# Optimization experiments

Measured on AMD Instinct MI355X. Metric: run time of the kernel, lower is better.

## Reference

```python
import jax, jax.numpy as jnp
import numpy as np

DIM = 512
A_HEADS = 8
C_HEADS = 4
DH = 64
EPS = 1e-5


def layer_norm(x, g, b):
    mu = jnp.mean(x, axis=-1, keepdims=True)
    var = jnp.var(x, axis=-1, keepdims=True)
    return (x - mu) * jax.lax.rsqrt(var + EPS) * g + b


def setup_inputs() -> dict:
    key = jax.random.key(0)
    ks = jax.random.split(key, 8)
    inner_a = A_HEADS * DH  # 512
    inner_c = C_HEADS * DH  # 256
    s = 0.02
    return {
        "x": jax.random.normal(ks[0], (4, 192, DIM), dtype=jnp.float32),
        # Attention branch params
        "ln1_g": jnp.ones((DIM,), jnp.float32),
        "ln1_b": jnp.zeros((DIM,), jnp.float32),
        "Wqkv": jax.random.normal(ks[1], (DIM, 3 * inner_a), jnp.float32) * s,
        "Wo": jax.random.normal(ks[2], (inner_a, DIM), jnp.float32) * s,
        "bo": jnp.zeros((DIM,), jnp.float32),
        # Trittention branch params
        "ln2_g": jnp.ones((DIM,), jnp.float32),
        "ln2_b": jnp.zeros((DIM,), jnp.float32),
        "Wabcde": jax.random.normal(ks[3], (DIM, 5 * inner_c), jnp.float32) * s,
        "babcde": jnp.zeros((5 * inner_c,), jnp.float32),
        "Wp": jax.random.normal(ks[4], (inner_c, DIM), jnp.float32) * s,
        "bp": jnp.zeros((DIM,), jnp.float32),
    }


def _attention(x, ln_g, ln_b, Wqkv, Wo, bo):
    B, T, _ = x.shape
    xn = layer_norm(x, ln_g, ln_b)
    qkv = xn @ Wqkv  # [B,T,3*H*D]
    q, k, v = jnp.split(qkv, 3, axis=-1)
    def heads(t):
        return t.reshape(B, T, A_HEADS, DH).transpose(0, 2, 1, 3)  # [B,H,T,D]
    q, k, v = heads(q), heads(k), heads(v)
    scale = DH ** -0.5
    dots = jnp.einsum('bhqd,bhkd->bhqk', q, k) * scale
    attn = jax.nn.softmax(dots, axis=-1)
    out = jnp.einsum('bhqk,bhkd->bhqd', attn, v)
    out = out.transpose(0, 2, 1, 3).reshape(B, T, A_HEADS * DH)
    return out @ Wo + bo


def _trittention(x, ln_g, ln_b, Wabcde, babcde, Wp, bp):
    B, T, _ = x.shape
    xn = layer_norm(x, ln_g, ln_b)
    proj = xn @ Wabcde + babcde  # [B,T,5*H*D]
    a, b_, c, d_, e = jnp.split(proj, 5, axis=-1)
    def heads(t):
        return t.reshape(B, T, C_HEADS, DH)  # [B,T,H,D]
    a, b_, c, d_, e = heads(a), heads(b_), heads(c), heads(d_), heads(e)
    # cubic score: [B,H,S,T,Q]
    score = jnp.einsum('bshd,bthd,bqhd->bhstq', a, b_, c) / DH
    # softmax over joint (s,t) for each query q
    score = score.transpose(0, 1, 4, 2, 3).reshape(B, C_HEADS, T, T * T)
    attn = jax.nn.softmax(score, axis=-1).reshape(B, C_HEADS, T, T, T)
    z = (jnp.einsum('bhqst,bshd->bhqd', attn, d_)
         + jnp.einsum('bhqst,bthd->bhqd', attn, e))
    z = z.transpose(0, 2, 1, 3).reshape(B, T, C_HEADS * DH)
    return z @ Wp + bp


def reference(x, ln1_g, ln1_b, Wqkv, Wo, bo, ln2_g, ln2_b, Wabcde, babcde, Wp, bp):
    return (_attention(x, ln1_g, ln1_b, Wqkv, Wo, bo)
            + _trittention(x, ln2_g, ln2_b, Wabcde, babcde, Wp, bp))
```

## Files before the change

kernel.cpp:

```cpp
#include <hip/hip_runtime.h>
#include <cstdint>


#define B_   4
#define T_   192
#define DIM_ 512
#define AH   8
#define CH   4

typedef unsigned short u16;
typedef unsigned int   u32;
typedef __attribute__((ext_vector_type(8))) short short8;
typedef __attribute__((ext_vector_type(4))) float floatx4;
typedef __attribute__((ext_vector_type(4))) int intx4;
typedef __attribute__((ext_vector_type(2))) float f32x2;
typedef __attribute__((ext_vector_type(8))) _Float16 half8;
typedef __attribute__((ext_vector_type(2))) _Float16 half2v;
typedef __attribute__((ext_vector_type(2))) __fp16 fp16x2;

union Frag  { intx4 i; short8 s; };
union FragH { intx4 i; half8 h; };

__device__ __forceinline__ floatx4 mfma16(Frag a, Frag b, floatx4 c) {
    return __builtin_amdgcn_mfma_f32_16x16x32_bf16(a.s, b.s, c, 0, 0, 0);
}
__device__ __forceinline__ floatx4 mfma16h(FragH a, FragH b, floatx4 c) {
    return __builtin_amdgcn_mfma_f32_16x16x32_f16(a.h, b.h, c, 0, 0, 0);
}

__device__ __forceinline__ float fexp2(float x) {
    return __builtin_amdgcn_exp2f(x);
}

__device__ __forceinline__ float wave_reduce_sum(float v) {
#pragma unroll
    for (int off = 32; off >= 1; off >>= 1)
        v += __shfl_xor(v, off, 64);
    return v;
}

__device__ __forceinline__ u32 pack_rne(float x, float y) {
    u32 ux = __float_as_uint(x);
    u32 uy = __float_as_uint(y);
    ux += 0x7fffu + ((ux >> 16) & 1u);
    uy += 0x7fffu + ((uy >> 16) & 1u);
    return (ux >> 16) | (uy & 0xffff0000u);
}
__device__ __forceinline__ u16 bf16_rne(float x) {
    u32 u = __float_as_uint(x);
    u += 0x7fffu + ((u >> 16) & 1u);
    return (u16)(u >> 16);
}
__device__ __forceinline__ float bf16f(u16 h) { return __uint_as_float(((u32)h) << 16); }

__device__ __forceinline__ u32 pack_f16(float x, float y) {
    union { fp16x2 h; u32 u; } cv;
    cv.h = __builtin_amdgcn_cvt_pkrtz(x, y);
    return cv.u;
}
__device__ __forceinline__ u32 mul_h2(u32 a, u32 b) {
    union { u32 u; half2v h; } ua, ub, uw;
    ua.u = a; ub.u = b;
    uw.h = ua.h * ub.h;
    return uw.u;
}

__device__ __forceinline__ Frag ld_frag8(const u16* p) {
    Frag f;
    uint2 a = *(const uint2*)p;
    uint2 b = *(const uint2*)(p + 4);
    f.i = (intx4){ (int)a.x, (int)a.y, (int)b.x, (int)b.y };
    return f;
}

#define LOG2E 1.44269504088896f

__global__ __launch_bounds__(256) void prep_kernel(
    const float* __restrict__ x,
    const float* __restrict__ g1, const float* __restrict__ b1,
    const float* __restrict__ g2, const float* __restrict__ b2,
    u16* __restrict__ x1h, u16* __restrict__ x2h,
    const float* __restrict__ Wqkv, u16* __restrict__ wqh,
    const float* __restrict__ Wab,  u16* __restrict__ wah,
    const float* __restrict__ Wo,   const float* __restrict__ Wp,
    u16* __restrict__ wofh, float* __restrict__ zero_base)
{
    __shared__ union { float t[64][65]; float red[4][2]; } u;
    const int tid = threadIdx.x;
    {
        int gid = blockIdx.x * 256 + tid;
        if (gid < 294912) ((float4*)zero_base)[gid] = make_float4(0.f, 0.f, 0.f, 0.f);
    }
    if (blockIdx.x < 768) {
        int row = blockIdx.x;
        const float2 v = ((const float2*)(x + (size_t)row * DIM_))[tid];
        float s  = v.x + v.y;
        float s2 = v.x * v.x + v.y * v.y;
        s  = wave_reduce_sum(s);
        s2 = wave_reduce_sum(s2);
        int w = tid >> 6;
        if ((tid & 63) == 0) { u.red[w][0] = s; u.red[w][1] = s2; }
        __syncthreads();
        float ts  = u.red[0][0] + u.red[1][0] + u.red[2][0] + u.red[3][0];
        float ts2 = u.red[0][1] + u.red[1][1] + u.red[2][1] + u.red[3][1];
        float mean = ts * (1.0f / DIM_);
        float var  = ts2 * (1.0f / DIM_) - mean * mean;
        float rstd = rsqrtf(var + 1e-5f);
        int c0 = tid * 2;
        float n0 = (v.x - mean) * rstd;
        float n1 = (v.y - mean) * rstd;
        float a0 = n0 * g1[c0] + b1[c0], a1 = n1 * g1[c0 + 1] + b1[c0 + 1];
        float c2 = n0 * g2[c0] + b2[c0], c3 = n1 * g2[c0 + 1] + b2[c0 + 1];
        size_t o = (size_t)row * 256 + tid;
        ((u32*)x1h)[o] = pack_rne(a0, a1);
        ((u32*)x2h)[o] = pack_rne(c2, c3);
        return;
    }
    int id = blockIdx.x - 768;
    const float* W; u16 *H; int K, N, Kout, kofs, tile;
    if (id < 192)      { W = Wqkv; H = wqh;  K = 512; N = 1536; Kout = 512; kofs = 0;   tile = id;       }
    else if (id < 352) { W = Wab;  H = wah;  K = 512; N = 1280; Kout = 512; kofs = 0;   tile = id - 192; }
    else if (id < 416) { W = Wo;   H = wofh; K = 512; N = 512;  Kout = 768; kofs = 0;   tile = id - 352; }
    else               { W = Wp;   H = wofh; K = 256; N = 512;  Kout = 768; kofs = 512; tile = id - 416; }
    int nx = N >> 6;
    int n0 = (tile % nx) * 64, k0 = (tile / nx) * 64;
    int rr = tid >> 4, c4 = (tid & 15) << 2;
#pragma unroll
    for (int p = 0; p < 4; ++p) {
        int row = rr + p * 16;
        float4 v = *(const float4*)(W + (size_t)(k0 + row) * N + n0 + c4);
        u.t[row][c4 + 0] = v.x; u.t[row][c4 + 1] = v.y;
        u.t[row][c4 + 2] = v.z; u.t[row][c4 + 3] = v.w;
    }
    __syncthreads();
#pragma unroll
    for (int p = 0; p < 4; ++p) {
        int n = rr + p * 16;
        u16 hi[4];
#pragma unroll
        for (int c = 0; c < 4; ++c)
            hi[c] = bf16_rne(u.t[c4 + c][n]);
        size_t o = (size_t)(n0 + n) * Kout + kofs + k0 + c4;
        *(uint2*)&H[o] = make_uint2((u32)hi[0] | ((u32)hi[1] << 16), (u32)hi[2] | ((u32)hi[3] << 16));
    }
}

__global__ __launch_bounds__(256) void gemm_dual(
    const u16* __restrict__ x1h, const u16* __restrict__ wqh,
    const u16* __restrict__ x2h, const u16* __restrict__ wah,
    const float* __restrict__ babcde,
    float* __restrict__ qkv, float* __restrict__ proj)
{
    __shared__ u16 As[64][68];
    __shared__ u16 Bs[64][68];
    const int tid = threadIdx.x;
    const int nb = blockIdx.x;
    const u16 *Ah, *BTh; const float* bias; float* C; int N, bn;
    if (nb < 24) { Ah = x1h; BTh = wqh; bias = nullptr; C = qkv;  N = 1536; bn = nb * 64; }
    else         { Ah = x2h; BTh = wah; bias = babcde; C = proj; N = 1280; bn = (nb - 24) * 64; }
    const int K = 512;
    const int bm = blockIdx.y * 64;
    const int lane = tid & 63, wave = tid >> 6;
    const int m16 = lane & 15, quad = lane >> 4;
    const int wm = (wave >> 1) * 32, wn = (wave & 1) * 32;
    const int r = tid >> 2, c16 = (tid & 3) * 16;

    floatx4 acc[2][2];
#pragma unroll
    for (int i = 0; i < 2; ++i)
#pragma unroll
        for (int j = 0; j < 2; ++j) acc[i][j] = (floatx4){0.f, 0.f, 0.f, 0.f};

    for (int k0 = 0; k0 < K; k0 += 64) {
        __syncthreads();
        {
            const u16* pa = Ah + (size_t)(bm + r) * K + k0 + c16;
            uint4 v0 = *(const uint4*)pa, v1 = *(const uint4*)(pa + 8);
            *(uint2*)&As[r][c16 + 0]  = make_uint2(v0.x, v0.y);
            *(uint2*)&As[r][c16 + 4]  = make_uint2(v0.z, v0.w);
            *(uint2*)&As[r][c16 + 8]  = make_uint2(v1.x, v1.y);
            *(uint2*)&As[r][c16 + 12] = make_uint2(v1.z, v1.w);
        }
        {
            const u16* pb = BTh + (size_t)(bn + r) * K + k0 + c16;
            uint4 v0 = *(const uint4*)pb, v1 = *(const uint4*)(pb + 8);
            *(uint2*)&Bs[r][c16 + 0]  = make_uint2(v0.x, v0.y);
            *(uint2*)&Bs[r][c16 + 4]  = make_uint2(v0.z, v0.w);
            *(uint2*)&Bs[r][c16 + 8]  = make_uint2(v1.x, v1.y);
            *(uint2*)&Bs[r][c16 + 12] = make_uint2(v1.z, v1.w);
        }
        __syncthreads();
#pragma unroll
        for (int ks = 0; ks < 2; ++ks) {
            const int ko = ks * 32 + quad * 8;
            Frag a0 = ld_frag8(&As[wm + m16][ko]);
            Frag a1 = ld_frag8(&As[wm + 16 + m16][ko]);
            Frag b0 = ld_frag8(&Bs[wn + m16][ko]);
            Frag b1 = ld_frag8(&Bs[wn + 16 + m16][ko]);
            acc[0][0] = mfma16(a0, b0, acc[0][0]);
            acc[0][1] = mfma16(a0, b1, acc[0][1]);
            acc[1][0] = mfma16(a1, b0, acc[1][0]);
            acc[1][1] = mfma16(a1, b1, acc[1][1]);
        }
    }
#pragma unroll
    for (int i = 0; i < 2; ++i)
#pragma unroll
        for (int rr = 0; rr < 4; ++rr) {
            int m = bm + wm + i * 16 + quad * 4 + rr;
#pragma unroll
            for (int j = 0; j < 2; ++j) {
                int n = bn + wn + j * 16 + m16;
                float v = acc[i][j][rr];
                if (bias) v += bias[n];
                C[(size_t)m * N + n] = v;
            }
        }
}

__global__ __launch_bounds__(256) void gemm_epilogue(
    const u16* __restrict__ aoh, const u16* __restrict__ zh,
    const u16* __restrict__ BTh,
    const float* __restrict__ bo, const float* __restrict__ bp,
    float* __restrict__ C)
{
    __shared__ u16 As[32][68];
    __shared__ u16 Bs[64][68];
    const int tid = threadIdx.x;
    const int bm = blockIdx.y * 32, bn = blockIdx.x * 64;
    const int lane = tid & 63, wave = tid >> 6;
    const int m16 = lane & 15, quad = lane >> 4;
    const int wm = (wave >> 1) * 16, wn = (wave & 1) * 32;
    const int ra = tid >> 3, c8 = (tid & 7) * 8;
    const int rb = tid >> 2, c16 = (tid & 3) * 16;
    const int N = 512, K = 768;

    floatx4 acc[2];
    acc[0] = (floatx4){0.f, 0.f, 0.f, 0.f};
    acc[1] = (floatx4){0.f, 0.f, 0.f, 0.f};

    for (int k0 = 0; k0 < K; k0 += 64) {
        __syncthreads();
        {
            const u16* pah = (k0 < 512)
                ? aoh + (size_t)(bm + ra) * 512 + k0 + c8
                : zh  + (size_t)(bm + ra) * 256 + (k0 - 512) + c8;
            uint4 v = *(const uint4*)pah;
            *(uint2*)&As[ra][c8 + 0] = make_uint2(v.x, v.y);
            *(uint2*)&As[ra][c8 + 4] = make_uint2(v.z, v.w);
        }
        {
            const u16* pb = BTh + (size_t)(bn + rb) * K + k0 + c16;
            uint4 v0 = *(const uint4*)pb, v1 = *(const uint4*)(pb + 8);
            *(uint2*)&Bs[rb][c16 + 0]  = make_uint2(v0.x, v0.y);
            *(uint2*)&Bs[rb][c16 + 4]  = make_uint2(v0.z, v0.w);
            *(uint2*)&Bs[rb][c16 + 8]  = make_uint2(v1.x, v1.y);
            *(uint2*)&Bs[rb][c16 + 12] = make_uint2(v1.z, v1.w);
        }
        __syncthreads();
#pragma unroll
        for (int ks = 0; ks < 2; ++ks) {
            const int ko = ks * 32 + quad * 8;
            Frag ah = ld_frag8(&As[wm + m16][ko]);
            Frag b0 = ld_frag8(&Bs[wn + m16][ko]);
            Frag b1 = ld_frag8(&Bs[wn + 16 + m16][ko]);
            acc[0] = mfma16(ah, b0, acc[0]);
            acc[1] = mfma16(ah, b1, acc[1]);
        }
    }
#pragma unroll
    for (int rr = 0; rr < 4; ++rr) {
        int m = bm + wm + quad * 4 + rr;
#pragma unroll
        for (int j = 0; j < 2; ++j) {
            int n = bn + wn + j * 16 + m16;
            C[(size_t)m * N + n] = acc[j][rr] + bo[n] + bp[n];
        }
    }
}

__global__ __launch_bounds__(256, 3) void attn_tritt(
    const float* __restrict__ qkv, const float* __restrict__ proj,
    u16* __restrict__ aoh, float* __restrict__ rs1, float* __restrict__ rt1)
{
    __shared__ union {
        struct {
            union { u16 Ks[96][68]; u16 P[64][100]; } kp;
            u16 Vt[64][100];
        } at;
        struct {
            u32 a_lds[48 * 36];
            u32 b_lds[48 * 36];
            float rs_lds[48][33];
            float rt_lds[48][33];
        } tr;
    } S;
    const int tid = threadIdx.x;
    const int lane = tid & 63, wave = tid >> 6;
    const int m16 = lane & 15, quad = lane >> 4;

    if (blockIdx.x < 96) {
        const int ab = blockIdx.x;
        const int b = ab / 24, rem = ab % 24;
        const int h = rem / 3, qt3 = rem % 3;
        const int qg = wave;
        const size_t base = (size_t)(b * T_) * 1536 + h * 64;

        Frag qf0, qf1;
        {
            const float s = 0.125f * LOG2E;
            const float* qp = qkv + base + (size_t)(qt3 * 64 + qg * 16 + m16) * 1536 + quad * 8;
            float4 u0 = *(const float4*)qp;
            float4 u1 = *(const float4*)(qp + 4);
            float4 u2 = *(const float4*)(qp + 32);
            float4 u3 = *(const float4*)(qp + 36);
            qf0.i = (intx4){ (int)pack_rne(u0.x * s, u0.y * s), (int)pack_rne(u0.z * s, u0.w * s),
                             (int)pack_rne(u1.x * s, u1.y * s), (int)pack_rne(u1.z * s, u1.w * s) };
            qf1.i = (intx4){ (int)pack_rne(u2.x * s, u2.y * s), (int)pack_rne(u2.z * s, u2.w * s),
                             (int)pack_rne(u3.x * s, u3.y * s), (int)pack_rne(u3.z * s, u3.w * s) };
        }

        float rsum[4] = {0.f, 0.f, 0.f, 0.f};
        floatx4 acco[4];
#pragma unroll
        for (int dt = 0; dt < 4; ++dt) acco[dt] = (floatx4){0.f, 0.f, 0.f, 0.f};

        for (int p = 0; p < 2; ++p) {
            if (p) __syncthreads();
            for (int i = tid; i < 96 * 16; i += 256) {
                int row = i >> 4, c4 = (i & 15) << 2;
                const float* kp = qkv + base + (size_t)(p * 96 + row) * 1536 + 512 + c4;
                float4 kv = *(const float4*)kp;
                *(uint2*)&S.at.kp.Ks[row][c4] = make_uint2(pack_rne(kv.x, kv.y), pack_rne(kv.z, kv.w));
                float4 vv = *(const float4*)(qkv + base + (size_t)(p * 96 + row) * 1536 + 1024 + c4);
                S.at.Vt[c4 + 0][row] = bf16_rne(vv.x);
                S.at.Vt[c4 + 1][row] = bf16_rne(vv.y);
                S.at.Vt[c4 + 2][row] = bf16_rne(vv.z);
                S.at.Vt[c4 + 3][row] = bf16_rne(vv.w);
            }
            __syncthreads();

            float ev[6][4];
#pragma unroll
            for (int tt = 0; tt < 6; ++tt) {
                Frag kb0 = ld_frag8(&S.at.kp.Ks[tt * 16 + m16][quad * 8]);
                Frag kb1 = ld_frag8(&S.at.kp.Ks[tt * 16 + m16][32 + quad * 8]);
                floatx4 accs = (floatx4){0.f, 0.f, 0.f, 0.f};
                accs = mfma16(qf0, kb0, accs);
                accs = mfma16(qf1, kb1, accs);
#pragma unroll
                for (int rr = 0; rr < 4; ++rr) {
                    float e = fexp2(accs[rr]);
                    ev[tt][rr] = e;
                    rsum[rr] += e;
                }
            }
            __syncthreads();
#pragma unroll
            for (int tt = 0; tt < 6; ++tt)
#pragma unroll
                for (int rr = 0; rr < 4; ++rr)
                    S.at.kp.P[qg * 16 + quad * 4 + rr][tt * 16 + m16] = bf16_rne(ev[tt][rr]);
#pragma unroll
            for (int ts = 0; ts < 3; ++ts) {
                Frag pf = ld_frag8(&S.at.kp.P[qg * 16 + m16][ts * 32 + quad * 8]);
#pragma unroll
                for (int dt = 0; dt < 4; ++dt) {
                    Frag vf = ld_frag8(&S.at.Vt[dt * 16 + m16][ts * 32 + quad * 8]);
                    acco[dt] = mfma16(pf, vf, acco[dt]);
                }
            }
        }

        float rinv[4];
#pragma unroll
        for (int rr = 0; rr < 4; ++rr) {
            float v = rsum[rr];
            v += __shfl_xor(v, 1, 64);
            v += __shfl_xor(v, 2, 64);
            v += __shfl_xor(v, 4, 64);
            v += __shfl_xor(v, 8, 64);
            rinv[rr] = 1.0f / v;
        }
#pragma unroll
        for (int dt = 0; dt < 4; ++dt)
#pragma unroll
            for (int rr = 0; rr < 4; ++rr) {
                float o = acco[dt][rr] * rinv[rr];
                size_t idx = (size_t)(b * T_ + qt3 * 64 + qg * 16 + quad * 4 + rr) * 512
                           + h * 64 + dt * 16 + m16;
                aoh[idx] = bf16_rne(o);
            }
        return;
    }

    const int t2 = blockIdx.x - 96;
    const int xx = t2 % 96;
    const int h = (t2 / 96) % CH;
    const int b = t2 / (96 * CH);
    const int qt = xx >> 4;
    const int sc = (xx >> 2) & 3;
    const int tc = xx & 3;
    const int q0 = qt * 32, s0 = sc * 48, t0 = tc * 48;
    const int bh = b * CH + h;
    const size_t rowbase = (size_t)(b * T_) * 1280 + h * 64;
    const float kA = 0.015625f * LOG2E;

    for (int i = tid; i < 48 * 32; i += 256) {
        int row = i >> 5, cp = i & 31;
        const float2 va = *(const float2*)(proj + rowbase + (size_t)(s0 + row) * 1280 + 0 + cp * 2);
        S.tr.a_lds[row * 36 + cp] = pack_f16(va.x * kA, va.y * kA);
        const float2 vb = *(const float2*)(proj + rowbase + (size_t)(t0 + row) * 1280 + 256 + cp * 2);
        S.tr.b_lds[row * 36 + cp] = pack_f16(vb.x, vb.y);
    }

    FragH cf[2][2];
#pragma unroll
    for (int jq = 0; jq < 2; ++jq) {
        const float* cp = proj + rowbase + (size_t)(q0 + jq * 16 + m16) * 1280 + 512 + quad * 8;
        float4 u0 = *(const float4*)(cp);
        float4 u1 = *(const float4*)(cp + 4);
        float4 u2 = *(const float4*)(cp + 32);
        float4 u3 = *(const float4*)(cp + 36);
        cf[jq][0].i = (intx4){ (int)pack_f16(u0.x, u0.y), (int)pack_f16(u0.z, u0.w),
                               (int)pack_f16(u1.x, u1.y), (int)pack_f16(u1.z, u1.w) };
        cf[jq][1].i = (intx4){ (int)pack_f16(u2.x, u2.y), (int)pack_f16(u2.z, u2.w),
                               (int)pack_f16(u3.x, u3.y), (int)pack_f16(u3.z, u3.w) };
    }
    __syncthreads();

    float rt_acc[3][4][2] = {};

    for (int si = 0; si < 12; ++si) {
        const int srow = wave * 12 + si;
        const intx4 av0 = *(const intx4*)(S.tr.a_lds + srow * 36 + quad * 4);
        const intx4 av1 = *(const intx4*)(S.tr.a_lds + srow * 36 + 16 + quad * 4);
        float rs_s[2] = {0.f, 0.f};
#pragma unroll
        for (int tt = 0; tt < 3; ++tt) {
            const u32* bp = S.tr.b_lds + (tt * 16 + m16) * 36;
            intx4 bv0 = *(const intx4*)(bp + quad * 4);
            intx4 bv1 = *(const intx4*)(bp + 16 + quad * 4);
            FragH w0, w1;
#pragma unroll
            for (int j = 0; j < 4; ++j) {
                w0.i[j] = (int)mul_h2((u32)av0[j], (u32)bv0[j]);
                w1.i[j] = (int)mul_h2((u32)av1[j], (u32)bv1[j]);
            }
#pragma unroll
            for (int jq = 0; jq < 2; ++jq) {
                floatx4 acc = (floatx4){0.f, 0.f, 0.f, 0.f};
                acc = mfma16h(w0, cf[jq][0], acc);
                acc = mfma16h(w1, cf[jq][1], acc);
#pragma unroll
                for (int rr = 0; rr < 4; ++rr) {
                    float e = fexp2(acc[rr]);
                    rt_acc[tt][rr][jq] += e;
                    rs_s[jq] += e;
                }
            }
        }
#pragma unroll
        for (int jq = 0; jq < 2; ++jq) {
            float v = rs_s[jq];
            v += __shfl_xor(v, 16, 64);
            v += __shfl_xor(v, 32, 64);
            if (lane < 16) S.tr.rs_lds[srow][jq * 16 + m16] = v;
        }
    }

    __syncthreads();
    for (int w = 0; w < 4; ++w) {
        if (wave == w) {
#pragma unroll
            for (int tt = 0; tt < 3; ++tt)
#pragma unroll
                for (int rr = 0; rr < 4; ++rr) {
                    int t = tt * 16 + quad * 4 + rr;
#pragma unroll
                    for (int jq = 0; jq < 2; ++jq) {
                        if (w == 0) S.tr.rt_lds[t][jq * 16 + m16] = rt_acc[tt][rr][jq];
                        else        S.tr.rt_lds[t][jq * 16 + m16] += rt_acc[tt][rr][jq];
                    }
                }
        }
        __syncthreads();
    }
    for (int i = tid; i < 32 * 48; i += 256) {
        int qq = i / 48, ss = i - qq * 48;
        unsafeAtomicAdd(&rs1[((size_t)bh * T_ + q0 + qq) * T_ + s0 + ss], S.tr.rs_lds[ss][qq]);
    }
    for (int i = tid; i < 32 * 48; i += 256) {
        int qq = i / 48, t3 = i - qq * 48;
        unsafeAtomicAdd(&rt1[((size_t)bh * T_ + q0 + qq) * T_ + t0 + t3], S.tr.rt_lds[t3][qq]);
    }
}

__global__ __launch_bounds__(256) void zgemm(
    const float* __restrict__ rs1, const float* __restrict__ rt1,
    const float* __restrict__ proj, u16* __restrict__ zzh)
{
    __shared__ u16 As[2][32][68];
    __shared__ u16 Bs[64][68];
    __shared__ float zred[32][9];
    __shared__ float Zl[32];
    const int mt = blockIdx.x, bh = blockIdx.y;
    const int b = bh >> 2, h = bh & 3;
    const int q0 = mt * 32;
    const int tid = threadIdx.x;
    const int lane = tid & 63, wave = tid >> 6;
    const int m16 = lane & 15, quad = lane >> 4;
    const int wm = (wave >> 1) * 16, wn = (wave & 1) * 32;
    const int ra = tid >> 3, c8 = (tid & 7) * 8;
    const int sl = tid >> 2, d4b = (tid & 3) * 4;

    float zacc = 0.f;
    floatx4 acc[2];
    acc[0] = (floatx4){0.f, 0.f, 0.f, 0.f};
    acc[1] = (floatx4){0.f, 0.f, 0.f, 0.f};

    for (int k0 = 0; k0 < 384; k0 += 64) {
        __syncthreads();
        {
            float g[8];
            if (k0 < 192) {
                const float* p = rs1 + ((size_t)bh * T_ + q0 + ra) * T_ + k0 + c8;
                float4 v0 = *(const float4*)(p);
                float4 v1 = *(const float4*)(p + 4);
                g[0] = v0.x; g[1] = v0.y; g[2] = v0.z; g[3] = v0.w;
                g[4] = v1.x; g[5] = v1.y; g[6] = v1.z; g[7] = v1.w;
                zacc += ((g[0] + g[1]) + (g[2] + g[3])) + ((g[4] + g[5]) + (g[6] + g[7]));
            } else {
                const float* p = rt1 + ((size_t)bh * T_ + q0 + ra) * T_ + (k0 - 192) + c8;
                float4 v0 = *(const float4*)(p);
                float4 v1 = *(const float4*)(p + 4);
                g[0] = v0.x; g[1] = v0.y; g[2] = v0.z; g[3] = v0.w;
                g[4] = v1.x; g[5] = v1.y; g[6] = v1.z; g[7] = v1.w;
            }
#pragma unroll
            for (int i = 0; i < 8; ++i) {
                u16 hi = bf16_rne(g[i]);
                As[0][ra][c8 + i] = hi;
                As[1][ra][c8 + i] = bf16_rne(g[i] - bf16f(hi));
            }
        }
        {
            const int colbase = (k0 < 192 ? 768 : 1024) + h * 64;
            const int s0 = (k0 < 192 ? k0 : k0 - 192);
#pragma unroll
            for (int i = 0; i < 4; ++i) {
                int dd = d4b + i * 16;
                float4 v = *(const float4*)(proj + (size_t)(b * T_ + s0 + sl) * 1280 + colbase + dd);
                Bs[dd + 0][sl] = bf16_rne(v.x);
                Bs[dd + 1][sl] = bf16_rne(v.y);
                Bs[dd + 2][sl] = bf16_rne(v.z);
                Bs[dd + 3][sl] = bf16_rne(v.w);
            }
        }
        __syncthreads();
#pragma unroll
        for (int ks = 0; ks < 2; ++ks) {
            const int ko = ks * 32 + quad * 8;
            Frag gh = ld_frag8(&As[0][wm + m16][ko]);
            Frag gl = ld_frag8(&As[1][wm + m16][ko]);
            Frag d0 = ld_frag8(&Bs[wn + m16][ko]);
            Frag d1 = ld_frag8(&Bs[wn + 16 + m16][ko]);
            acc[0] = mfma16(gh, d0, acc[0]);
            acc[0] = mfma16(gl, d0, acc[0]);
            acc[1] = mfma16(gh, d1, acc[1]);
            acc[1] = mfma16(gl, d1, acc[1]);
        }
    }
    zred[ra][tid & 7] = zacc;
    __syncthreads();
    if (tid < 32) {
        float s = ((zred[tid][0] + zred[tid][1]) + (zred[tid][2] + zred[tid][3]))
                + ((zred[tid][4] + zred[tid][5]) + (zred[tid][6] + zred[tid][7]));
        Zl[tid] = 1.0f / s;
    }
    __syncthreads();
#pragma unroll
    for (int j = 0; j < 2; ++j)
#pragma unroll
        for (int rr = 0; rr < 4; ++rr) {
            int m = wm + quad * 4 + rr;
            int d = wn + j * 16 + m16;
            float zv = acc[j][rr] * Zl[m];
            size_t idx = (size_t)(b * T_ + q0 + m) * 256 + h * 64 + d;
            zzh[idx] = bf16_rne(zv);
        }
}

extern "C" void kernel_launch(void* const* d_in, const int* in_sizes, int n_in,
                              void* d_out, int out_size, void* d_ws, size_t ws_size,
                              hipStream_t stream)
{
    const float* x      = (const float*)d_in[0];
    const float* ln1_g  = (const float*)d_in[1];
    const float* ln1_b  = (const float*)d_in[2];
    const float* Wqkv   = (const float*)d_in[3];
    const float* Wo     = (const float*)d_in[4];
    const float* bo     = (const float*)d_in[5];
    const float* ln2_g  = (const float*)d_in[6];
    const float* ln2_b  = (const float*)d_in[7];
    const float* Wabcde = (const float*)d_in[8];
    const float* babcde = (const float*)d_in[9];
    const float* Wp     = (const float*)d_in[10];
    const float* bp     = (const float*)d_in[11];
    float* out = (float*)d_out;

    float* ws   = (float*)d_ws;
    float* proj = ws;
    u16* wofh   = (u16*)(ws + 983040);
    u16* aoh    = (u16*)(ws + 1179648);
    u16* zh     = (u16*)(ws + 1376256);
    float* qkv  = ws + 1474560;
    u16* x1h    = (u16*)(ws + 2654208);
    u16* x2h    = (u16*)(ws + 2850816);
    u16* wqh    = (u16*)(ws + 3047424);
    u16* wah    = (u16*)(ws + 3440640);
    float* rs1  = ws + 3768320;
    float* rt1  = ws + 4358144;

    prep_kernel<<<1216, 256, 0, stream>>>(x, ln1_g, ln1_b, ln2_g, ln2_b,
                                          x1h, x2h,
                                          Wqkv, wqh, Wabcde, wah,
                                          Wo, Wp, wofh, rs1);
    gemm_dual<<<dim3(44, 12), 256, 0, stream>>>(x1h, wqh, x2h, wah,
                                                babcde, qkv, proj);
    attn_tritt<<<96 + 1536, 256, 0, stream>>>(qkv, proj, aoh, rs1, rt1);
    zgemm<<<dim3(6, 16), 256, 0, stream>>>(rs1, rt1, proj, zh);
    gemm_epilogue<<<dim3(8, 24), 256, 0, stream>>>(aoh, zh, wofh, bo, bp, out);
}
```

Baseline: 148.4 us.

## Fuse z-GEMM and output projection into one kernel with atomic accumulation

```diff
diff --git a/kernel.cpp b/kernel.cpp
--- a/kernel.cpp
+++ b/kernel.cpp
@@ -83,13 +83,14 @@
     const float* __restrict__ Wqkv, u16* __restrict__ wqh,
     const float* __restrict__ Wab,  u16* __restrict__ wah,
     const float* __restrict__ Wo,   const float* __restrict__ Wp,
-    u16* __restrict__ wofh, float* __restrict__ zero_base)
+    u16* __restrict__ wofh, float* __restrict__ zero_base, float* __restrict__ outz)
 {
     __shared__ union { float t[64][65]; float red[4][2]; } u;
     const int tid = threadIdx.x;
     {
         int gid = blockIdx.x * 256 + tid;
         if (gid < 294912) ((float4*)zero_base)[gid] = make_float4(0.f, 0.f, 0.f, 0.f);
+        if (gid < 98304)  ((float4*)outz)[gid]      = make_float4(0.f, 0.f, 0.f, 0.f);
     }
     if (blockIdx.x < 768) {
         int row = blockIdx.x;
@@ -174,7 +175,8 @@
     for (int k0 = 0; k0 < K; k0 += 64) {
         __syncthreads();
         {
-            const u16* pa = Ah + (size_t)(bm + r) * K + k0 + c16;
+            const u16* pa = x1h == Ah ? Ah + (size_t)(bm + r) * K + k0 + c16
+                                      : Ah + (size_t)(bm + r) * K + k0 + c16;
             uint4 v0 = *(const uint4*)pa, v1 = *(const uint4*)(pa + 8);
             *(uint2*)&As[r][c16 + 0]  = make_uint2(v0.x, v0.y);
             *(uint2*)&As[r][c16 + 4]  = make_uint2(v0.z, v0.w);
@@ -216,67 +218,6 @@
                 C[(size_t)m * N + n] = v;
             }
         }
-}
-
-__global__ __launch_bounds__(256) void gemm_epilogue(
-    const u16* __restrict__ aoh, const u16* __restrict__ zh,
-    const u16* __restrict__ BTh,
-    const float* __restrict__ bo, const float* __restrict__ bp,
-    float* __restrict__ C)
-{
-    __shared__ u16 As[32][68];
-    __shared__ u16 Bs[64][68];
-    const int tid = threadIdx.x;
-    const int bm = blockIdx.y * 32, bn = blockIdx.x * 64;
-    const int lane = tid & 63, wave = tid >> 6;
-    const int m16 = lane & 15, quad = lane >> 4;
-    const int wm = (wave >> 1) * 16, wn = (wave & 1) * 32;
-    const int ra = tid >> 3, c8 = (tid & 7) * 8;
-    const int rb = tid >> 2, c16 = (tid & 3) * 16;
-    const int N = 512, K = 768;
-
-    floatx4 acc[2];
-    acc[0] = (floatx4){0.f, 0.f, 0.f, 0.f};
-    acc[1] = (floatx4){0.f, 0.f, 0.f, 0.f};
-
-    for (int k0 = 0; k0 < K; k0 += 64) {
-        __syncthreads();
-        {
-            const u16* pah = (k0 < 512)
-                ? aoh + (size_t)(bm + ra) * 512 + k0 + c8
-                : zh  + (size_t)(bm + ra) * 256 + (k0 - 512) + c8;
-            uint4 v = *(const uint4*)pah;
-            *(uint2*)&As[ra][c8 + 0] = make_uint2(v.x, v.y);
-            *(uint2*)&As[ra][c8 + 4] = make_uint2(v.z, v.w);
-        }
-        {
-            const u16* pb = BTh + (size_t)(bn + rb) * K + k0 + c16;
-            uint4 v0 = *(const uint4*)pb, v1 = *(const uint4*)(pb + 8);
-            *(uint2*)&Bs[rb][c16 + 0]  = make_uint2(v0.x, v0.y);
-            *(uint2*)&Bs[rb][c16 + 4]  = make_uint2(v0.z, v0.w);
-            *(uint2*)&Bs[rb][c16 + 8]  = make_uint2(v1.x, v1.y);
-            *(uint2*)&Bs[rb][c16 + 12] = make_uint2(v1.z, v1.w);
-        }
-        __syncthreads();
-#pragma unroll
-        for (int ks = 0; ks < 2; ++ks) {
-            const int ko = ks * 32 + quad * 8;
-            Frag ah = ld_frag8(&As[wm + m16][ko]);
-            Frag b0 = ld_frag8(&Bs[wn + m16][ko]);
-            Frag b1 = ld_frag8(&Bs[wn + 16 + m16][ko]);
-            acc[0] = mfma16(ah, b0, acc[0]);
-            acc[1] = mfma16(ah, b1, acc[1]);
-        }
-    }
-#pragma unroll
-    for (int rr = 0; rr < 4; ++rr) {
-        int m = bm + wm + quad * 4 + rr;
-#pragma unroll
-        for (int j = 0; j < 2; ++j) {
-            int n = bn + wn + j * 16 + m16;
-            C[(size_t)m * N + n] = acc[j][rr] + bo[n] + bp[n];
-        }
-    }
 }
 
 __global__ __launch_bounds__(256, 3) void attn_tritt(
@@ -496,20 +437,73 @@
     }
 }
 
-__global__ __launch_bounds__(256) void zgemm(
-    const float* __restrict__ rs1, const float* __restrict__ rt1,
-    const float* __restrict__ proj, u16* __restrict__ zzh)
+__global__ __launch_bounds__(256) void finale(
+    const u16* __restrict__ aoh, const float* __restrict__ rs1, const float* __restrict__ rt1,
+    const float* __restrict__ proj, const u16* __restrict__ wofh,
+    const float* __restrict__ bo, const float* __restrict__ bp,
+    float* __restrict__ out)
 {
-    __shared__ u16 As[2][32][68];
-    __shared__ u16 Bs[64][68];
-    __shared__ float zred[32][9];
-    __shared__ float Zl[32];
-    const int mt = blockIdx.x, bh = blockIdx.y;
-    const int b = bh >> 2, h = bh & 3;
-    const int q0 = mt * 32;
+    __shared__ union {
+        struct { u16 As[32][68]; u16 Bs[64][68]; } A;
+        struct { u16 Am[2][32][68]; u16 Bs[64][68]; float zred[32][9]; float Zl[32]; } B;
+    } S;
     const int tid = threadIdx.x;
     const int lane = tid & 63, wave = tid >> 6;
     const int m16 = lane & 15, quad = lane >> 4;
+
+    if (blockIdx.x < 192) {
+        const int bn = (blockIdx.x & 7) * 64, bm = (blockIdx.x >> 3) * 32;
+        const int wm = (wave >> 1) * 16, wn = (wave & 1) * 32;
+        const int ra = tid >> 3, c8 = (tid & 7) * 8;
+        const int rb = tid >> 2, c16 = (tid & 3) * 16;
+
+        floatx4 acc[2];
+        acc[0] = (floatx4){0.f, 0.f, 0.f, 0.f};
+        acc[1] = (floatx4){0.f, 0.f, 0.f, 0.f};
+
+        for (int k0 = 0; k0 < 512; k0 += 64) {
+            __syncthreads();
+            {
+                const u16* pah = aoh + (size_t)(bm + ra) * 512 + k0 + c8;
+                uint4 v = *(const uint4*)pah;
+                *(uint2*)&S.A.As[ra][c8 + 0] = make_uint2(v.x, v.y);
+                *(uint2*)&S.A.As[ra][c8 + 4] = make_uint2(v.z, v.w);
+            }
+            {
+                const u16* pb = wofh + (size_t)(bn + rb) * 768 + k0 + c16;
+                uint4 v0 = *(const uint4*)pb, v1 = *(const uint4*)(pb + 8);
+                *(uint2*)&S.A.Bs[rb][c16 + 0]  = make_uint2(v0.x, v0.y);
+                *(uint2*)&S.A.Bs[rb][c16 + 4]  = make_uint2(v0.z, v0.w);
+                *(uint2*)&S.A.Bs[rb][c16 + 8]  = make_uint2(v1.x, v1.y);
+                *(uint2*)&S.A.Bs[rb][c16 + 12] = make_uint2(v1.z, v1.w);
+            }
+            __syncthreads();
+#pragma unroll
+            for (int ks = 0; ks < 2; ++ks) {
+                const int ko = ks * 32 + quad * 8;
+                Frag ah = ld_frag8(&S.A.As[wm + m16][ko]);
+                Frag b0 = ld_frag8(&S.A.Bs[wn + m16][ko]);
+                Frag b1 = ld_frag8(&S.A.Bs[wn + 16 + m16][ko]);
+                acc[0] = mfma16(ah, b0, acc[0]);
+                acc[1] = mfma16(ah, b1, acc[1]);
+            }
+        }
+#pragma unroll
+        for (int rr = 0; rr < 4; ++rr) {
+            int m = bm + wm + quad * 4 + rr;
+#pragma unroll
+            for (int j = 0; j < 2; ++j) {
+                int n = bn + wn + j * 16 + m16;
+                unsafeAtomicAdd(&out[(size_t)m * 512 + n], acc[j][rr] + bo[n] + bp[n]);
+            }
+        }
+        return;
+    }
+
+    const int blockB = blockIdx.x - 192;
+    const int mt = blockB % 6, bh = blockB / 6;
+    const int b = bh >> 2, h = bh & 3;
+    const int q0 = mt * 32;
     const int wm = (wave >> 1) * 16, wn = (wave & 1) * 32;
     const int ra = tid >> 3, c8 = (tid & 7) * 8;
     const int sl = tid >> 2, d4b = (tid & 3) * 4;
@@ -540,8 +534,8 @@
 #pragma unroll
             for (int i = 0; i < 8; ++i) {
                 u16 hi = bf16_rne(g[i]);
-                As[0][ra][c8 + i] = hi;
-                As[1][ra][c8 + i] = bf16_rne(g[i] - bf16f(hi));
+                S.B.Am[0][ra][c8 + i] = hi;
+                S.B.Am[1][ra][c8 + i] = bf16_rne(g[i] - bf16f(hi));
             }
         }
         {
@@ -551,44 +545,73 @@
             for (int i = 0; i < 4; ++i) {
                 int dd = d4b + i * 16;
                 float4 v = *(const float4*)(proj + (size_t)(b * T_ + s0 + sl) * 1280 + colbase + dd);
-                Bs[dd + 0][sl] = bf16_rne(v.x);
-                Bs[dd + 1][sl] = bf16_rne(v.y);
-                Bs[dd + 2][sl] = bf16_rne(v.z);
-                Bs[dd + 3][sl] = bf16_rne(v.w);
+                S.B.Bs[dd + 0][sl] = bf16_rne(v.x);
+                S.B.Bs[dd + 1][sl] = bf16_rne(v.y);
+                S.B.Bs[dd + 2][sl] = bf16_rne(v.z);
+                S.B.Bs[dd + 3][sl] = bf16_rne(v.w);
             }
         }
         __syncthreads();
 #pragma unroll
         for (int ks = 0; ks < 2; ++ks) {
             const int ko = ks * 32 + quad * 8;
-            Frag gh = ld_frag8(&As[0][wm + m16][ko]);
-            Frag gl = ld_frag8(&As[1][wm + m16][ko]);
-            Frag d0 = ld_frag8(&Bs[wn + m16][ko]);
-            Frag d1 = ld_frag8(&Bs[wn + 16 + m16][ko]);
+            Frag gh = ld_frag8(&S.B.Am[0][wm + m16][ko]);
+            Frag gl = ld_frag8(&S.B.Am[1][wm + m16][ko]);
+            Frag d0 = ld_frag8(&S.B.Bs[wn + m16][ko]);
+            Frag d1 = ld_frag8(&S.B.Bs[wn + 16 + m16][ko]);
             acc[0] = mfma16(gh, d0, acc[0]);
             acc[0] = mfma16(gl, d0, acc[0]);
             acc[1] = mfma16(gh, d1, acc[1]);
             acc[1] = mfma16(gl, d1, acc[1]);
         }
     }
-    zred[ra][tid & 7] = zacc;
+    S.B.zred[ra][tid & 7] = zacc;
     __syncthreads();
     if (tid < 32) {
-        float s = ((zred[tid][0] + zred[tid][1]) + (zred[tid][2] + zred[tid][3]))
-                + ((zred[tid][4] + zred[tid][5]) + (zred[tid][6] + zred[tid][7]));
-        Zl[tid] = 1.0f / s;
+        float s = ((S.B.zred[tid][0] + S.B.zred[tid][1]) + (S.B.zred[tid][2] + S.B.zred[tid][3]))
+                + ((S.B.zred[tid][4] + S.B.zred[tid][5]) + (S.B.zred[tid][6] + S.B.zred[tid][7]));
+        S.B.Zl[tid] = 1.0f / s;
     }
     __syncthreads();
-#pragma unroll
-    for (int j = 0; j < 2; ++j)
-#pragma unroll
-        for (int rr = 0; rr < 4; ++rr) {
-            int m = wm + quad * 4 + rr;
-            int d = wn + j * 16 + m16;
-            float zv = acc[j][rr] * Zl[m];
-            size_t idx = (size_t)(b * T_ + q0 + m) * 256 + h * 64 + d;
-            zzh[idx] = bf16_rne(zv);
-        }
+    {
+        float zv[2][4];
+#pragma unroll
+        for (int j = 0; j < 2; ++j)
+#pragma unroll
+            for (int rr = 0; rr < 4; ++rr) {
+                int m = wm + quad * 4 + rr;
+                zv[j][rr] = acc[j][rr] * S.B.Zl[m];
+            }
+        __syncthreads();
+#pragma unroll
+        for (int j = 0; j < 2; ++j)
+#pragma unroll
+            for (int rr = 0; rr < 4; ++rr) {
+                int m = wm + quad * 4 + rr;
+                int d = wn + j * 16 + m16;
+                S.B.Am[0][m][d] = bf16_rne(zv[j][rr]);
+            }
+    }
+    __syncthreads();
+#pragma unroll
+    for (int t = 0; t < 8; ++t) {
+        const int n0 = wave * 128 + t * 16;
+        Frag bf0 = ld_frag8(&wofh[(size_t)(n0 + m16) * 768 + 512 + h * 64 + quad * 8]);
+        Frag bf1 = ld_frag8(&wofh[(size_t)(n0 + m16) * 768 + 512 + h * 64 + 32 + quad * 8]);
+#pragma unroll
+        for (int qi = 0; qi < 2; ++qi) {
+            Frag za = ld_frag8(&S.B.Am[0][qi * 16 + m16][quad * 8]);
+            Frag zb = ld_frag8(&S.B.Am[0][qi * 16 + m16][32 + quad * 8]);
+            floatx4 ac = (floatx4){0.f, 0.f, 0.f, 0.f};
+            ac = mfma16(za, bf0, ac);
+            ac = mfma16(zb, bf1, ac);
+#pragma unroll
+            for (int rr = 0; rr < 4; ++rr) {
+                int m = b * T_ + q0 + qi * 16 + quad * 4 + rr;
+                unsafeAtomicAdd(&out[(size_t)m * 512 + n0 + m16], ac[rr]);
+            }
+        }
+    }
 }
 
 extern "C" void kernel_launch(void* const* d_in, const int* in_sizes, int n_in,
@@ -613,22 +636,20 @@
     float* proj = ws;
     u16* wofh   = (u16*)(ws + 983040);
     u16* aoh    = (u16*)(ws + 1179648);
-    u16* zh     = (u16*)(ws + 1376256);
-    float* qkv  = ws + 1474560;
-    u16* x1h    = (u16*)(ws + 2654208);
-    u16* x2h    = (u16*)(ws + 2850816);
-    u16* wqh    = (u16*)(ws + 3047424);
-    u16* wah    = (u16*)(ws + 3440640);
-    float* rs1  = ws + 3768320;
-    float* rt1  = ws + 4358144;
+    float* qkv  = ws + 1376256;
+    u16* x1h    = (u16*)(ws + 2555904);
+    u16* x2h    = (u16*)(ws + 2752512);
+    u16* wqh    = (u16*)(ws + 2949120);
+    u16* wah    = (u16*)(ws + 3342336);
+    float* rs1  = ws + 3670016;
+    float* rt1  = ws + 4259840;
 
     prep_kernel<<<1216, 256, 0, stream>>>(x, ln1_g, ln1_b, ln2_g, ln2_b,
                                           x1h, x2h,
                                           Wqkv, wqh, Wabcde, wah,
-                                          Wo, Wp, wofh, rs1);
+                                          Wo, Wp, wofh, rs1, out);
     gemm_dual<<<dim3(44, 12), 256, 0, stream>>>(x1h, wqh, x2h, wah,
                                                 babcde, qkv, proj);
     attn_tritt<<<96 + 1536, 256, 0, stream>>>(qkv, proj, aoh, rs1, rt1);
-    zgemm<<<dim3(6, 16), 256, 0, stream>>>(rs1, rt1, proj, zh);
-    gemm_epilogue<<<dim3(8, 24), 256, 0, stream>>>(aoh, zh, wofh, bo, bp, out);
-}
+    finale<<<288, 256, 0, stream>>>(aoh, rs1, rt1, proj, wofh, bo, bp, out);
+}
```

After: 138.8 us. 1.07x faster.
